# Performance work log

Measured on AMD Instinct MI355X. Metric: run time of the kernel, lower is better.

Reference implementation:

```python
import jax, jax.numpy as jnp
import numpy as np

PE_DIM = 64

def _layernorm(x, g, b, eps=1e-5):
    m = jnp.mean(x, -1, keepdims=True)
    v = jnp.mean((x - m) ** 2, -1, keepdims=True)
    return (x - m) * jax.lax.rsqrt(v + eps) * g + b

def _sinusoidal_pe(t, dim=PE_DIM):
    half = dim // 2
    freqs = jnp.exp(-jnp.log(10000.0) * jnp.arange(half) / half).astype(t.dtype)
    ang = t[..., None] * freqs  # [..., half]
    return jnp.concatenate([jnp.sin(ang), jnp.cos(ang)], -1)

def _bilinear(feats, b, t, x, y):
    # feats [B,Wl,H,W,D]; b,t int32 [B,Q,Wl,M] (b broadcastable); x,y in [0,1]
    # matches torch grid_sample(mode=bilinear, padding_mode=border, align_corners=False)
    H, W = feats.shape[2], feats.shape[3]
    px = x * W - 0.5
    py = y * H - 0.5
    x0 = jnp.floor(px); y0 = jnp.floor(py)
    wx = (px - x0)[..., None]; wy = (py - y0)[..., None]
    x0i = jnp.clip(x0.astype(jnp.int32), 0, W - 1)
    x1i = jnp.clip(x0.astype(jnp.int32) + 1, 0, W - 1)
    y0i = jnp.clip(y0.astype(jnp.int32), 0, H - 1)
    y1i = jnp.clip(y0.astype(jnp.int32) + 1, 0, H - 1)
    v00 = feats[b, t, y0i, x0i]  # [B,Q,Wl,M,D]
    v01 = feats[b, t, y0i, x1i]
    v10 = feats[b, t, y1i, x0i]
    v11 = feats[b, t, y1i, x1i]
    return (v00 * (1 - wy) * (1 - wx) + v01 * (1 - wy) * wx
            + v10 * wy * (1 - wx) + v11 * wy * wx)

def setup_inputs() -> dict:
    key = jax.random.key(0)
    ks = jax.random.split(key, 20)
    B, Q, Wl, H, W, D, M = 4, 300, 8, 64, 64, 256, 4
    s = 0.02
    inp = {
        'q': jax.random.normal(ks[0], (B, Q, D), jnp.float32),
        'kv_feats': jax.random.normal(ks[1], (B, Wl, H, W, D), jnp.float32),
        'kv_mask': jnp.zeros((B, Wl, H, W), jnp.bool_),
        'delta_sec': jax.random.normal(ks[2], (B, Q, Wl), jnp.float32),
        'w_ref': jax.random.normal(ks[3], (D, 2), jnp.float32) * s,
        'b_ref': jnp.zeros((2,), jnp.float32),
        'w_delta': jax.random.normal(ks[4], (2 * D, 3 * M), jnp.float32) * s,
        'b_delta': jnp.zeros((3 * M,), jnp.float32),
        'w_alpha': jax.random.normal(ks[5], (2 * D, M), jnp.float32) * s,
        'b_alpha': jnp.zeros((M,), jnp.float32),
        'lam': jnp.array(1.0, jnp.float32),
        'w_proj': jax.random.normal(ks[6], (D, D), jnp.float32) * s,
        'b_proj': jnp.zeros((D,), jnp.float32),
        'ln1_g': jnp.ones((D,), jnp.float32), 'ln1_b': jnp.zeros((D,), jnp.float32),
        'ln2_g': jnp.ones((D,), jnp.float32), 'ln2_b': jnp.zeros((D,), jnp.float32),
        'w_ffn1': jax.random.normal(ks[7], (D, 4 * D), jnp.float32) * s,
        'b_ffn1': jnp.zeros((4 * D,), jnp.float32),
        'w_ffn2': jax.random.normal(ks[8], (4 * D, D), jnp.float32) * s,
        'b_ffn2': jnp.zeros((D,), jnp.float32),
        'w_rel': jax.random.normal(ks[9], (PE_DIM, D), jnp.float32) * s,
        'b_rel': jnp.zeros((D,), jnp.float32),
    }
    return inp

def reference(q, kv_feats, kv_mask, delta_sec, w_ref, b_ref, w_delta, b_delta,
              w_alpha, b_alpha, lam, w_proj, b_proj, ln1_g, ln1_b, ln2_g, ln2_b,
              w_ffn1, b_ffn1, w_ffn2, b_ffn2, w_rel, b_rel):
    B, Q, D = q.shape
    Wl = kv_feats.shape[1]
    M = w_alpha.shape[1]

    qn = _layernorm(q, ln1_g, ln1_b)
    rel_feat = _sinusoidal_pe(delta_sec) @ w_rel + b_rel          # [B,Q,Wl,D]
    psi = jnp.concatenate([jnp.broadcast_to(qn[:, :, None, :], (B, Q, Wl, D)),
                           rel_feat], -1)                          # [B,Q,Wl,2D]

    delta = (psi @ w_delta + b_delta).reshape(B, Q, Wl, M, 3)
    logits = psi @ w_alpha + b_alpha                               # [B,Q,Wl,M]
    ref = jax.nn.sigmoid(qn @ w_ref + b_ref)                       # [B,Q,2]
    coords = ref[:, :, None, None, :] + jnp.tanh(delta[..., :2])   # [B,Q,Wl,M,2]
    coords = jnp.clip(coords, 0.0, 1.0)
    delta_t = jnp.tanh(delta[..., 2])                              # [B,Q,Wl,M]

    # mask features (mask==True -> invalid -> zero)
    feats = kv_feats * (~kv_mask)[..., None].astype(kv_feats.dtype)

    # temporal trilinear indices
    base = jnp.arange(Wl, dtype=q.dtype).reshape(1, 1, Wl, 1)
    target = base + delta_t
    t0f = jnp.clip(jnp.floor(target), 0, Wl - 1)
    t1f = jnp.clip(t0f + 1, 0, Wl - 1)
    alpha = (target - t0f)[..., None]
    t0 = t0f.astype(jnp.int32); t1 = t1f.astype(jnp.int32)

    bidx = jnp.arange(B, dtype=jnp.int32).reshape(B, 1, 1, 1)
    cx = coords[..., 0]; cy = coords[..., 1]
    s0 = _bilinear(feats, bidx, t0, cx, cy)                        # [B,Q,Wl,M,D]
    s1 = _bilinear(feats, bidx, t1, cx, cy)
    sampled = s0 * (1 - alpha) + s1 * alpha

    lam_sp = jax.nn.softplus(lam)
    weights = jax.nn.softmax(logits - lam_sp * jnp.abs(delta_sec)[..., None], axis=-1)
    agg = jnp.sum(weights[..., None] * sampled, axis=(2, 3))       # [B,Q,D]

    out = q + (agg @ w_proj + b_proj)
    h = _layernorm(out, ln2_g, ln2_b)
    ffn = jax.nn.gelu(h @ w_ffn1 + b_ffn1, approximate=False) @ w_ffn2 + b_ffn2
    return out + ffn
```

## Files before the change

kernel.cpp:

```cpp
#include <hip/hip_runtime.h>
#include <math.h>

#define Bn 4
#define Qn 300
#define WL 8
#define Hh 64
#define Ww 64
#define Dd 256
#define Mm 4

__device__ __forceinline__ float wave_reduce(float v) {
#pragma unroll
    for (int off = 32; off > 0; off >>= 1) v += __shfl_down(v, off, 64);
    return v;
}

__device__ __forceinline__ float lo16(unsigned u) { return __uint_as_float(u << 16); }
__device__ __forceinline__ float hi16(unsigned u) { return __uint_as_float(u & 0xffff0000u); }

__device__ __forceinline__ unsigned bfp(float a, float b) {
    unsigned ua = __float_as_uint(a); ua = (ua + 0x7fffu + ((ua >> 16) & 1u)) >> 16;
    unsigned ub = __float_as_uint(b); ub = (ub + 0x7fffu + ((ub >> 16) & 1u)) >> 16;
    return ua | (ub << 16);
}

__device__ __forceinline__ void unpack8(uint4 wv, float* w) {
    w[0] = lo16(wv.x); w[1] = hi16(wv.x); w[2] = lo16(wv.y); w[3] = hi16(wv.y);
    w[4] = lo16(wv.z); w[5] = hi16(wv.z); w[6] = lo16(wv.w); w[7] = hi16(wv.w);
}

__device__ __forceinline__ float dot8(float4 ha, float4 hb, const float* w) {
    return ha.x * w[0] + ha.y * w[1] + ha.z * w[2] + ha.w * w[3]
         + hb.x * w[4] + hb.y * w[5] + hb.z * w[6] + hb.w * w[7];
}

__global__ void __launch_bounds__(512, 4) k_front(const float* __restrict__ wp,
                                                  const float* __restrict__ wf1,
                                                  const float* __restrict__ wf2,
                                                  unsigned* __restrict__ pk,
                                                  const float* __restrict__ q,
                                                  const float* __restrict__ g1,
                                                  const float* __restrict__ b1,
                                                  const float* __restrict__ w_ref,
                                                  const float* __restrict__ b_ref,
                                                  const float* __restrict__ dsec,
                                                  const float* __restrict__ w_rel,
                                                  const float* __restrict__ b_rel,
                                                  const float* __restrict__ w_delta,
                                                  const float* __restrict__ b_delta,
                                                  const float* __restrict__ w_alpha,
                                                  const float* __restrict__ b_alpha,
                                                  const unsigned char* __restrict__ mask,
                                                  const float* __restrict__ feats,
                                                  float* __restrict__ agg) {
    int bid = blockIdx.x, t = threadIdx.x;

    if (bid < 576) {
        int i = bid * 512 + t;
        if (i < 32768) {
            int p = i & 3, c = (i >> 2) & 255, g = i >> 10;
            pk[i] = bfp(wp[(g * 8 + 2 * p) * 256 + c], wp[(g * 8 + 2 * p + 1) * 256 + c]);
        } else if (i < 163840) {
            int i2 = i - 32768;
            int p = i2 & 3, c = (i2 >> 2) & 1023, g = i2 >> 12;
            pk[i] = bfp(wf1[(g * 8 + 2 * p) * 1024 + c], wf1[(g * 8 + 2 * p + 1) * 1024 + c]);
        } else {
            int i3 = i - 163840;
            int p = i3 & 3, c = (i3 >> 2) & 255, g = i3 >> 10;
            pk[i] = bfp(wf2[(g * 8 + 2 * p) * 256 + c], wf2[(g * 8 + 2 * p + 1) * 256 + c]);
        }
        return;
    }

    __shared__ float sqn[256];
    __shared__ float pe[8][64];
    __shared__ float rel[8][260];
    __shared__ __align__(16) float WcT[16 * 516];
    __shared__ float dres[2][8][16];
    __shared__ float res[8][16];
    __shared__ float red[16];
    __shared__ float sref[2];
    float (*part)[256] = (float (*)[256])WcT;
    unsigned* Prec = (unsigned*)(WcT + 2048);

    int bq = bid - 576;
    int ch = t & 255;
    bool lo = t < 256;
    int lane = t & 63, wv = t >> 6;

    float wr[64];
#pragma unroll
    for (int k = 0; k < 64; k++) wr[k] = w_rel[k * Dd + ch];

    for (int u = t; u < 512 * 16; u += 512) {
        int k = u >> 4, jj = u & 15;
        float w = (jj < 12) ? w_delta[k * 12 + jj] : w_alpha[k * 4 + (jj - 12)];
        WcT[jj * 516 + k] = w;
    }

    float x = lo ? q[bq * Dd + ch] : 0.f;
    float sm = wave_reduce(x);
    if (lane == 0) red[wv] = sm;
    __syncthreads();
    float m = (red[0] + red[1] + red[2] + red[3] + red[4] + red[5] + red[6] + red[7]) * (1.f / Dd);
    __syncthreads();
    float dx = lo ? (x - m) : 0.f;
    float sv = wave_reduce(dx * dx);
    if (lane == 0) red[wv] = sv;
    __syncthreads();
    float v = (red[0] + red[1] + red[2] + red[3] + red[4] + red[5] + red[6] + red[7]) * (1.f / Dd);
    __syncthreads();
    float y = 0.f;
    if (lo) { y = dx * rsqrtf(v + 1e-5f) * g1[ch] + b1[ch]; sqn[ch] = y; }

    if (lo) {
        int wl = t >> 5, i2 = t & 31;
        float f = expf(-logf(10000.f) * (float)i2 * (1.f / 32.f));
        float a = dsec[bq * WL + wl] * f;
        pe[wl][i2] = sinf(a);
        pe[wl][i2 + 32] = cosf(a);
    }

    float c0 = lo ? y * w_ref[2 * ch] : 0.f;
    float c1 = lo ? y * w_ref[2 * ch + 1] : 0.f;
    c0 = wave_reduce(c0); c1 = wave_reduce(c1);
    if (lane == 0) { red[wv] = c0; red[8 + wv] = c1; }
    __syncthreads();
    if (t == 0) {
        float s0 = red[0] + red[1] + red[2] + red[3] + red[4] + red[5] + red[6] + red[7] + b_ref[0];
        float s1 = red[8] + red[9] + red[10] + red[11] + red[12] + red[13] + red[14] + red[15] + b_ref[1];
        sref[0] = 1.f / (1.f + expf(-s0));
        sref[1] = 1.f / (1.f + expf(-s1));
    }

    {
        float brl = b_rel[ch];
        int wh = t >> 8;
#pragma unroll
        for (int w2 = 0; w2 < 4; w2++) {
            int wl = wh * 4 + w2;
            const float4* p4 = (const float4*)&pe[wl][0];
            float r = brl;
#pragma unroll
            for (int k4 = 0; k4 < 16; k4++) {
                float4 p = p4[k4];
                r += p.x * wr[4 * k4] + p.y * wr[4 * k4 + 1]
                   + p.z * wr[4 * k4 + 2] + p.w * wr[4 * k4 + 3];
            }
            rel[wl][ch] = r;
        }
    }
    __syncthreads();

    if (t < 256) {
        int h = t >> 7, idx = t & 127, wl = idx >> 4, jj = idx & 15;
        const float4* wrow = (const float4*)&WcT[jj * 516 + h * 256];
        const float4* arow = h ? (const float4*)&rel[wl][0] : (const float4*)sqn;
        float s = 0.f;
#pragma unroll 8
        for (int k4 = 0; k4 < 64; k4++) {
            float4 a = arow[k4], w = wrow[k4];
            s += a.x * w.x + a.y * w.y + a.z * w.z + a.w * w.w;
        }
        dres[h][wl][jj] = s;
    }
    __syncthreads();
    if (t < 128) {
        int wl = t >> 4, jj = t & 15;
        res[wl][jj] = dres[0][wl][jj] + dres[1][wl][jj]
                    + ((jj < 12) ? b_delta[jj] : b_alpha[jj - 12]);
    }
    __syncthreads();

    if (t < 32) {
        int wl = t >> 2, mm = t & 3;
        float l0 = res[wl][12], l1 = res[wl][13], l2 = res[wl][14], l3 = res[wl][15];
        float mx = fmaxf(fmaxf(l0, l1), fmaxf(l2, l3));
        float inv = 1.f / (expf(l0 - mx) + expf(l1 - mx) + expf(l2 - mx) + expf(l3 - mx));
        float wgt = expf(res[wl][12 + mm] - mx) * inv;

        float cx = fminf(fmaxf(sref[0] + tanhf(res[wl][mm * 3 + 0]), 0.f), 1.f);
        float cy = fminf(fmaxf(sref[1] + tanhf(res[wl][mm * 3 + 1]), 0.f), 1.f);
        float tgt = (float)wl + tanhf(res[wl][mm * 3 + 2]);
        float t0f = fminf(fmaxf(floorf(tgt), 0.f), (float)(WL - 1));
        float t1f = fminf(t0f + 1.f, (float)(WL - 1));
        float alpha = tgt - t0f;
        float px = cx * (float)Ww - 0.5f, py = cy * (float)Hh - 0.5f;
        float fx = floorf(px), fy = floorf(py);
        float wx = px - fx, wy = py - fy;
        int X0 = (int)fminf(fmaxf(fx, 0.f), (float)(Ww - 1));
        int X1 = (int)fminf(fmaxf(fx + 1.f, 0.f), (float)(Ww - 1));
        int Y0 = (int)fminf(fmaxf(fy, 0.f), (float)(Hh - 1));
        int Y1 = (int)fminf(fmaxf(fy + 1.f, 0.f), (float)(Hh - 1));
        int T0 = (int)t0f, T1 = (int)t1f;

        float w00 = (1.f - wy) * (1.f - wx), w01 = (1.f - wy) * wx;
        float w10 = wy * (1.f - wx), w11 = wy * wx;
        float wt0 = wgt * (1.f - alpha), wt1 = wgt * alpha;

        int b = bq / Qn;
        int base0 = (b * WL + T0) * Hh;
        int base1 = (b * WL + T1) * Hh;
        int i00 = (base0 + Y0) * Ww + X0, i01 = (base0 + Y0) * Ww + X1;
        int i10 = (base0 + Y1) * Ww + X0, i11 = (base0 + Y1) * Ww + X1;
        int j00 = (base1 + Y0) * Ww + X0, j01 = (base1 + Y0) * Ww + X1;
        int j10 = (base1 + Y1) * Ww + X0, j11 = (base1 + Y1) * Ww + X1;

        unsigned* rec = &Prec[t * 16];
        rec[0] = __float_as_uint(wt0 * w00 * (mask[i00] ? 0.f : 1.f));
        rec[1] = __float_as_uint(wt0 * w01 * (mask[i01] ? 0.f : 1.f));
        rec[2] = __float_as_uint(wt0 * w10 * (mask[i10] ? 0.f : 1.f));
        rec[3] = __float_as_uint(wt0 * w11 * (mask[i11] ? 0.f : 1.f));
        rec[4] = __float_as_uint(wt1 * w00 * (mask[j00] ? 0.f : 1.f));
        rec[5] = __float_as_uint(wt1 * w01 * (mask[j01] ? 0.f : 1.f));
        rec[6] = __float_as_uint(wt1 * w10 * (mask[j10] ? 0.f : 1.f));
        rec[7] = __float_as_uint(wt1 * w11 * (mask[j11] ? 0.f : 1.f));
        rec[8] = i00; rec[9] = i01; rec[10] = i10; rec[11] = i11;
        rec[12] = j00; rec[13] = j01; rec[14] = j10; rec[15] = j11;
    }
    __syncthreads();

    {
        const float4* f4 = (const float4*)feats;
        int j = t >> 6;
        float4 acc = {0.f, 0.f, 0.f, 0.f};
#pragma unroll
        for (int p = 0; p < 4; p++) {
            const unsigned* rec = &Prec[(j * 4 + p) * 16];
#pragma unroll
            for (int cn = 0; cn < 8; cn++) {
                float w = __uint_as_float(rec[cn]);
                size_t idx = rec[8 + cn];
                float4 vv = f4[idx * 64 + lane];
                acc.x += w * vv.x; acc.y += w * vv.y; acc.z += w * vv.z; acc.w += w * vv.w;
            }
        }
        ((float4*)&part[j][0])[lane] = acc;
    }
    __syncthreads();
    if (t < 256) {
        agg[(size_t)bq * Dd + t] = part[0][t] + part[1][t] + part[2][t] + part[3][t]
                                 + part[4][t] + part[5][t] + part[6][t] + part[7][t];
    }
}

template<int R>
__device__ __forceinline__ void out_body(int row0,
        const float* __restrict__ q, const float* __restrict__ agg,
        const unsigned* __restrict__ pkP, const float* __restrict__ b_proj,
        const float* __restrict__ g2, const float* __restrict__ b2,
        const unsigned* __restrict__ pkF1, const float* __restrict__ b_ffn1,
        const unsigned* __restrict__ pkF2, const float* __restrict__ b_ffn2,
        float* __restrict__ out,
        float* sA, float* sO, float* sH, float* sF, float* sX, float* sRed) {
    int t = threadIdx.x;
    int j8 = t >> 7, c7 = t & 127;

    for (int u = t; u < 256 * R; u += 1024) {
        int r = u >> 8, cc = u & 255;
        sA[r * 256 + cc] = agg[(size_t)(row0 + r) * Dd + cc];
    }
    __syncthreads();

    {
        float a0[R], a1[R];
#pragma unroll
        for (int r = 0; r < R; r++) { a0[r] = 0.f; a1[r] = 0.f; }
#pragma unroll
        for (int gg = 0; gg < 4; gg++) {
            int g = j8 * 4 + gg;
            uint4 wv0 = *(const uint4*)&pkP[((unsigned)(g * 256 + c7)) * 4];
            uint4 wv1 = *(const uint4*)&pkP[((unsigned)(g * 256 + c7 + 128)) * 4];
            float w0[8], w1[8]; unpack8(wv0, w0); unpack8(wv1, w1);
#pragma unroll
            for (int r = 0; r < R; r++) {
                float4 ha = ((const float4*)&sA[r * 256])[g * 2];
                float4 hb = ((const float4*)&sA[r * 256])[g * 2 + 1];
                a0[r] += dot8(ha, hb, w0); a1[r] += dot8(ha, hb, w1);
            }
        }
#pragma unroll
        for (int r = 0; r < R; r++) {
            sX[(j8 * R + r) * 256 + c7] = a0[r];
            sX[(j8 * R + r) * 256 + c7 + 128] = a1[r];
        }
    }
    __syncthreads();

    for (int u = t; u < 256 * R; u += 1024) {
        int r = u >> 8, cc = u & 255;
        float o = q[(size_t)(row0 + r) * Dd + cc] + b_proj[cc];
#pragma unroll
        for (int jj = 0; jj < 8; jj++) o += sX[(jj * R + r) * 256 + cc];
        sO[r * 256 + cc] = o;
    }
    __syncthreads();

    {
        int wv = t >> 6, l = t & 63;
        if (wv < R) {
            float4 vv = ((const float4*)&sO[wv * 256])[l];
            float s = vv.x + vv.y + vv.z + vv.w;
            s = __shfl(wave_reduce(s), 0, 64);
            float mean = s * (1.f / 256.f);
            float d0 = vv.x - mean, d1 = vv.y - mean, d2 = vv.z - mean, d3 = vv.w - mean;
            float ss = d0 * d0 + d1 * d1 + d2 * d2 + d3 * d3;
            ss = __shfl(wave_reduce(ss), 0, 64);
            float rstd = rsqrtf(ss * (1.f / 256.f) + 1e-5f);
            if (l == 0) { sRed[wv * 2] = mean; sRed[wv * 2 + 1] = rstd; }
        }
    }
    __syncthreads();
    for (int u = t; u < 256 * R; u += 1024) {
        int r = u >> 8, cc = u & 255;
        sH[r * 256 + cc] = (sO[r * 256 + cc] - sRed[r * 2]) * sRed[r * 2 + 1] * g2[cc] + b2[cc];
    }
    __syncthreads();

    {
        int h = t >> 9, c2 = t & 511;
        float f0[R], f1[R];
#pragma unroll
        for (int r = 0; r < R; r++) { f0[r] = 0.f; f1[r] = 0.f; }
#pragma unroll 2
        for (int gg = 0; gg < 16; gg++) {
            int g = h * 16 + gg;
            uint4 wv0 = *(const uint4*)&pkF1[((unsigned)(g * 1024 + c2)) * 4];
            uint4 wv1 = *(const uint4*)&pkF1[((unsigned)(g * 1024 + c2 + 512)) * 4];
            float w0[8], w1[8]; unpack8(wv0, w0); unpack8(wv1, w1);
#pragma unroll
            for (int r = 0; r < R; r++) {
                float4 ha = ((const float4*)&sH[r * 256])[g * 2];
                float4 hb = ((const float4*)&sH[r * 256])[g * 2 + 1];
                f0[r] += dot8(ha, hb, w0); f1[r] += dot8(ha, hb, w1);
            }
        }
        float* dst = sX + h * (R * 1024);
#pragma unroll
        for (int r = 0; r < R; r++) {
            dst[r * 1024 + c2] = f0[r];
            dst[r * 1024 + c2 + 512] = f1[r];
        }
    }
    __syncthreads();
    {
        float bf = b_ffn1[t];
#pragma unroll
        for (int r = 0; r < R; r++) {
            float xx = sX[r * 1024 + t] + sX[R * 1024 + r * 1024 + t] + bf;
            sF[r * 1024 + t] = 0.5f * xx * (1.f + erff(xx * 0.70710678118654752f));
        }
    }
    __syncthreads();

    {
        float a0[R], a1[R];
#pragma unroll
        for (int r = 0; r < R; r++) { a0[r] = 0.f; a1[r] = 0.f; }
#pragma unroll 2
        for (int gg = 0; gg < 16; gg++) {
            int g = j8 * 16 + gg;
            uint4 wv0 = *(const uint4*)&pkF2[((unsigned)(g * 256 + c7)) * 4];
            uint4 wv1 = *(const uint4*)&pkF2[((unsigned)(g * 256 + c7 + 128)) * 4];
            float w0[8], w1[8]; unpack8(wv0, w0); unpack8(wv1, w1);
#pragma unroll
            for (int r = 0; r < R; r++) {
                float4 ha = ((const float4*)&sF[r * 1024])[g * 2];
                float4 hb = ((const float4*)&sF[r * 1024])[g * 2 + 1];
                a0[r] += dot8(ha, hb, w0); a1[r] += dot8(ha, hb, w1);
            }
        }
#pragma unroll
        for (int r = 0; r < R; r++) {
            sX[(j8 * R + r) * 256 + c7] = a0[r];
            sX[(j8 * R + r) * 256 + c7 + 128] = a1[r];
        }
    }
    __syncthreads();

    for (int u = t; u < 256 * R; u += 1024) {
        int r = u >> 8, cc = u & 255;
        float s = b_ffn2[cc];
#pragma unroll
        for (int jj = 0; jj < 8; jj++) s += sX[(jj * R + r) * 256 + cc];
        out[(size_t)(row0 + r) * Dd + cc] = sO[r * 256 + cc] + s;
    }
}

__global__ void __launch_bounds__(1024) k_out(const float* __restrict__ q,
                                              const float* __restrict__ agg,
                                              const unsigned* __restrict__ pkP,
                                              const float* __restrict__ b_proj,
                                              const float* __restrict__ g2,
                                              const float* __restrict__ b2,
                                              const unsigned* __restrict__ pkF1,
                                              const float* __restrict__ b_ffn1,
                                              const unsigned* __restrict__ pkF2,
                                              const float* __restrict__ b_ffn2,
                                              float* __restrict__ out) {
    __shared__ float sA[5 * 256];
    __shared__ float sO[5 * 256];
    __shared__ float sH[5 * 256];
    __shared__ float sF[5 * 1024];
    __shared__ float sX[10240];
    __shared__ float sRed[16];
    __shared__ float pad[1600];
    if (b_ffn2 == nullptr) pad[threadIdx.x & 1023] = 0.f;

    int bid = blockIdx.x;
    if (bid < 176) {
        out_body<5>(bid * 5, q, agg, pkP, b_proj, g2, b2, pkF1, b_ffn1, pkF2, b_ffn2,
                    out, sA, sO, sH, sF, sX, sRed);
    } else {
        out_body<4>(880 + (bid - 176) * 4, q, agg, pkP, b_proj, g2, b2, pkF1, b_ffn1,
                    pkF2, b_ffn2, out, sA, sO, sH, sF, sX, sRed);
    }
}

extern "C" void kernel_launch(void* const* d_in, const int* in_sizes, int n_in,
                              void* d_out, int out_size, void* d_ws, size_t ws_size,
                              hipStream_t stream) {
    const float* q        = (const float*)d_in[0];
    const float* kv_feats = (const float*)d_in[1];
    const unsigned char* kv_mask = (const unsigned char*)d_in[2];
    const float* delta_sec= (const float*)d_in[3];
    const float* w_ref    = (const float*)d_in[4];
    const float* b_ref    = (const float*)d_in[5];
    const float* w_delta  = (const float*)d_in[6];
    const float* b_delta  = (const float*)d_in[7];
    const float* w_alpha  = (const float*)d_in[8];
    const float* b_alpha  = (const float*)d_in[9];
    const float* w_proj   = (const float*)d_in[11];
    const float* b_proj   = (const float*)d_in[12];
    const float* ln1_g    = (const float*)d_in[13];
    const float* ln1_b    = (const float*)d_in[14];
    const float* ln2_g    = (const float*)d_in[15];
    const float* ln2_b    = (const float*)d_in[16];
    const float* w_ffn1   = (const float*)d_in[17];
    const float* b_ffn1   = (const float*)d_in[18];
    const float* w_ffn2   = (const float*)d_in[19];
    const float* b_ffn2   = (const float*)d_in[20];
    const float* w_rel    = (const float*)d_in[21];
    const float* b_rel    = (const float*)d_in[22];
    float* out = (float*)d_out;

    unsigned* pk   = (unsigned*)d_ws;
    unsigned* pkP  = pk;
    unsigned* pkF1 = pk + 32768;
    unsigned* pkF2 = pk + 163840;
    float*    agg  = (float*)(pk + 294912);

    const int BQ = Bn * Qn;
    k_front<<<dim3(576 + BQ), dim3(512), 0, stream>>>(w_proj, w_ffn1, w_ffn2, pk,
                                                      q, ln1_g, ln1_b, w_ref, b_ref,
                                                      delta_sec, w_rel, b_rel,
                                                      w_delta, b_delta, w_alpha, b_alpha,
                                                      kv_mask, kv_feats, agg);
    k_out<<<dim3(256), dim3(1024), 0, stream>>>(q, agg, pkP, b_proj, ln2_g, ln2_b,
                                                pkF1, b_ffn1, pkF2, b_ffn2, out);
}
```

Baseline: 294.4 us.

## Switch output MLP weights and activations to fp16 with packed dot2 accumulation

Weights for the projection and both FFN layers are now packed as fp16 pairs instead of bf16, and activations in shared memory are stored as packed fp16 too. The inner products use the fdot2 instruction (two fp16 multiplies accumulated into fp32) instead of unpacking to fp32 and doing scalar FMAs. The aim is fewer ALU ops in the k_out matmuls and smaller shared-memory traffic. The cost is fp16 range and rounding on activations, and the shared-memory pad is enlarged, presumably to keep occupancy the same.

Result: faster. 278.3 us (-5.5%).

```diff
diff --git a/kernel.cpp b/kernel.cpp
--- a/kernel.cpp
+++ b/kernel.cpp
@@ -15,23 +15,32 @@
     return v;
 }
 
-__device__ __forceinline__ float lo16(unsigned u) { return __uint_as_float(u << 16); }
-__device__ __forceinline__ float hi16(unsigned u) { return __uint_as_float(u & 0xffff0000u); }
-
-__device__ __forceinline__ unsigned bfp(float a, float b) {
-    unsigned ua = __float_as_uint(a); ua = (ua + 0x7fffu + ((ua >> 16) & 1u)) >> 16;
-    unsigned ub = __float_as_uint(b); ub = (ub + 0x7fffu + ((ub >> 16) & 1u)) >> 16;
-    return ua | (ub << 16);
-}
-
-__device__ __forceinline__ void unpack8(uint4 wv, float* w) {
-    w[0] = lo16(wv.x); w[1] = hi16(wv.x); w[2] = lo16(wv.y); w[3] = hi16(wv.y);
-    w[4] = lo16(wv.z); w[5] = hi16(wv.z); w[6] = lo16(wv.w); w[7] = hi16(wv.w);
-}
-
-__device__ __forceinline__ float dot8(float4 ha, float4 hb, const float* w) {
-    return ha.x * w[0] + ha.y * w[1] + ha.z * w[2] + ha.w * w[3]
-         + hb.x * w[4] + hb.y * w[5] + hb.z * w[6] + hb.w * w[7];
+using h2_t = _Float16 __attribute__((ext_vector_type(2)));
+
+__device__ __forceinline__ unsigned packh2(float a, float b) {
+    auto h = __builtin_amdgcn_cvt_pkrtz(a, b);
+    union { decltype(h) h; unsigned u; } x; x.h = h; return x.u;
+}
+
+__device__ __forceinline__ h2_t u2h2(unsigned u) {
+    union { unsigned u; h2_t h; } x; x.u = u; return x.h;
+}
+
+__device__ __forceinline__ float dot2p(unsigned a, unsigned w, float acc) {
+#if __has_builtin(__builtin_amdgcn_fdot2)
+    return __builtin_amdgcn_fdot2(u2h2(a), u2h2(w), acc, false);
+#else
+    h2_t A = u2h2(a), W = u2h2(w);
+    return acc + (float)A.x * (float)W.x + (float)A.y * (float)W.y;
+#endif
+}
+
+__device__ __forceinline__ float dot8h(uint4 av, uint4 wv, float acc) {
+    acc = dot2p(av.x, wv.x, acc);
+    acc = dot2p(av.y, wv.y, acc);
+    acc = dot2p(av.z, wv.z, acc);
+    acc = dot2p(av.w, wv.w, acc);
+    return acc;
 }
 
 __global__ void __launch_bounds__(512, 4) k_front(const float* __restrict__ wp,
@@ -59,15 +68,15 @@
         int i = bid * 512 + t;
         if (i < 32768) {
             int p = i & 3, c = (i >> 2) & 255, g = i >> 10;
-            pk[i] = bfp(wp[(g * 8 + 2 * p) * 256 + c], wp[(g * 8 + 2 * p + 1) * 256 + c]);
+            pk[i] = packh2(wp[(g * 8 + 2 * p) * 256 + c], wp[(g * 8 + 2 * p + 1) * 256 + c]);
         } else if (i < 163840) {
             int i2 = i - 32768;
             int p = i2 & 3, c = (i2 >> 2) & 1023, g = i2 >> 12;
-            pk[i] = bfp(wf1[(g * 8 + 2 * p) * 1024 + c], wf1[(g * 8 + 2 * p + 1) * 1024 + c]);
+            pk[i] = packh2(wf1[(g * 8 + 2 * p) * 1024 + c], wf1[(g * 8 + 2 * p + 1) * 1024 + c]);
         } else {
             int i3 = i - 163840;
             int p = i3 & 3, c = (i3 >> 2) & 255, g = i3 >> 10;
-            pk[i] = bfp(wf2[(g * 8 + 2 * p) * 256 + c], wf2[(g * 8 + 2 * p + 1) * 256 + c]);
+            pk[i] = packh2(wf2[(g * 8 + 2 * p) * 256 + c], wf2[(g * 8 + 2 * p + 1) * 256 + c]);
         }
         return;
     }
@@ -252,13 +261,14 @@
         const unsigned* __restrict__ pkF1, const float* __restrict__ b_ffn1,
         const unsigned* __restrict__ pkF2, const float* __restrict__ b_ffn2,
         float* __restrict__ out,
-        float* sA, float* sO, float* sH, float* sF, float* sX, float* sRed) {
+        unsigned* sA2, float* sO, unsigned* sH2, unsigned* sF2, float* sX, float* sRed) {
     int t = threadIdx.x;
     int j8 = t >> 7, c7 = t & 127;
 
-    for (int u = t; u < 256 * R; u += 1024) {
-        int r = u >> 8, cc = u & 255;
-        sA[r * 256 + cc] = agg[(size_t)(row0 + r) * Dd + cc];
+    for (int u = t; u < 128 * R; u += 1024) {
+        int r = u >> 7, c2 = u & 127;
+        float2 av = *(const float2*)&agg[(size_t)(row0 + r) * Dd + 2 * c2];
+        sA2[r * 128 + c2] = packh2(av.x, av.y);
     }
     __syncthreads();
 
@@ -271,12 +281,11 @@
             int g = j8 * 4 + gg;
             uint4 wv0 = *(const uint4*)&pkP[((unsigned)(g * 256 + c7)) * 4];
             uint4 wv1 = *(const uint4*)&pkP[((unsigned)(g * 256 + c7 + 128)) * 4];
-            float w0[8], w1[8]; unpack8(wv0, w0); unpack8(wv1, w1);
 #pragma unroll
             for (int r = 0; r < R; r++) {
-                float4 ha = ((const float4*)&sA[r * 256])[g * 2];
-                float4 hb = ((const float4*)&sA[r * 256])[g * 2 + 1];
-                a0[r] += dot8(ha, hb, w0); a1[r] += dot8(ha, hb, w1);
+                uint4 av = ((const uint4*)&sA2[r * 128])[g];
+                a0[r] = dot8h(av, wv0, a0[r]);
+                a1[r] = dot8h(av, wv1, a1[r]);
             }
         }
 #pragma unroll
@@ -311,45 +320,52 @@
         }
     }
     __syncthreads();
-    for (int u = t; u < 256 * R; u += 1024) {
-        int r = u >> 8, cc = u & 255;
-        sH[r * 256 + cc] = (sO[r * 256 + cc] - sRed[r * 2]) * sRed[r * 2 + 1] * g2[cc] + b2[cc];
-    }
-    __syncthreads();
-
-    {
-        int h = t >> 9, c2 = t & 511;
+    for (int u = t; u < 128 * R; u += 1024) {
+        int r = u >> 7, c2 = u & 127;
+        int cc = 2 * c2;
+        float mean = sRed[r * 2], rstd = sRed[r * 2 + 1];
+        float h0 = (sO[r * 256 + cc] - mean) * rstd * g2[cc] + b2[cc];
+        float h1 = (sO[r * 256 + cc + 1] - mean) * rstd * g2[cc + 1] + b2[cc + 1];
+        sH2[r * 128 + c2] = packh2(h0, h1);
+    }
+    __syncthreads();
+
+    {
+        int h = t >> 9, c2c = t & 511;
         float f0[R], f1[R];
 #pragma unroll
         for (int r = 0; r < R; r++) { f0[r] = 0.f; f1[r] = 0.f; }
 #pragma unroll 2
         for (int gg = 0; gg < 16; gg++) {
             int g = h * 16 + gg;
-            uint4 wv0 = *(const uint4*)&pkF1[((unsigned)(g * 1024 + c2)) * 4];
-            uint4 wv1 = *(const uint4*)&pkF1[((unsigned)(g * 1024 + c2 + 512)) * 4];
-            float w0[8], w1[8]; unpack8(wv0, w0); unpack8(wv1, w1);
+            uint4 wv0 = *(const uint4*)&pkF1[((unsigned)(g * 1024 + c2c)) * 4];
+            uint4 wv1 = *(const uint4*)&pkF1[((unsigned)(g * 1024 + c2c + 512)) * 4];
 #pragma unroll
             for (int r = 0; r < R; r++) {
-                float4 ha = ((const float4*)&sH[r * 256])[g * 2];
-                float4 hb = ((const float4*)&sH[r * 256])[g * 2 + 1];
-                f0[r] += dot8(ha, hb, w0); f1[r] += dot8(ha, hb, w1);
+                uint4 av = ((const uint4*)&sH2[r * 128])[g];
+                f0[r] = dot8h(av, wv0, f0[r]);
+                f1[r] = dot8h(av, wv1, f1[r]);
             }
         }
         float* dst = sX + h * (R * 1024);
 #pragma unroll
         for (int r = 0; r < R; r++) {
-            dst[r * 1024 + c2] = f0[r];
-            dst[r * 1024 + c2 + 512] = f1[r];
-        }
-    }
-    __syncthreads();
-    {
-        float bf = b_ffn1[t];
-#pragma unroll
-        for (int r = 0; r < R; r++) {
-            float xx = sX[r * 1024 + t] + sX[R * 1024 + r * 1024 + t] + bf;
-            sF[r * 1024 + t] = 0.5f * xx * (1.f + erff(xx * 0.70710678118654752f));
-        }
+            dst[r * 1024 + c2c] = f0[r];
+            dst[r * 1024 + c2c + 512] = f1[r];
+        }
+    }
+    __syncthreads();
+
+    for (int u = t; u < 512 * R; u += 1024) {
+        int r = u >> 9, p = u & 511;
+        float2 pa = ((const float2*)&sX[r * 1024])[p];
+        float2 pb = ((const float2*)&sX[R * 1024 + r * 1024])[p];
+        float2 bf = *(const float2*)&b_ffn1[2 * p];
+        float x0 = pa.x + pb.x + bf.x;
+        float x1 = pa.y + pb.y + bf.y;
+        float e0 = 0.5f * x0 * (1.f + erff(x0 * 0.70710678118654752f));
+        float e1 = 0.5f * x1 * (1.f + erff(x1 * 0.70710678118654752f));
+        sF2[r * 512 + p] = packh2(e0, e1);
     }
     __syncthreads();
 
@@ -362,12 +378,11 @@
             int g = j8 * 16 + gg;
             uint4 wv0 = *(const uint4*)&pkF2[((unsigned)(g * 256 + c7)) * 4];
             uint4 wv1 = *(const uint4*)&pkF2[((unsigned)(g * 256 + c7 + 128)) * 4];
-            float w0[8], w1[8]; unpack8(wv0, w0); unpack8(wv1, w1);
 #pragma unroll
             for (int r = 0; r < R; r++) {
-                float4 ha = ((const float4*)&sF[r * 1024])[g * 2];
-                float4 hb = ((const float4*)&sF[r * 1024])[g * 2 + 1];
-                a0[r] += dot8(ha, hb, w0); a1[r] += dot8(ha, hb, w1);
+                uint4 av = ((const uint4*)&sF2[r * 512])[g];
+                a0[r] = dot8h(av, wv0, a0[r]);
+                a1[r] = dot8h(av, wv1, a1[r]);
             }
         }
 #pragma unroll
@@ -398,22 +413,22 @@
                                               const unsigned* __restrict__ pkF2,
                                               const float* __restrict__ b_ffn2,
                                               float* __restrict__ out) {
-    __shared__ float sA[5 * 256];
-    __shared__ float sO[5 * 256];
-    __shared__ float sH[5 * 256];
-    __shared__ float sF[5 * 1024];
-    __shared__ float sX[10240];
+    __shared__ __align__(16) unsigned sA2[5 * 128];
+    __shared__ __align__(16) float sO[5 * 256];
+    __shared__ __align__(16) unsigned sH2[5 * 128];
+    __shared__ __align__(16) unsigned sF2[5 * 512];
+    __shared__ __align__(16) float sX[10240];
     __shared__ float sRed[16];
-    __shared__ float pad[1600];
+    __shared__ float pad[5120];
     if (b_ffn2 == nullptr) pad[threadIdx.x & 1023] = 0.f;
 
     int bid = blockIdx.x;
     if (bid < 176) {
         out_body<5>(bid * 5, q, agg, pkP, b_proj, g2, b2, pkF1, b_ffn1, pkF2, b_ffn2,
-                    out, sA, sO, sH, sF, sX, sRed);
+                    out, sA2, sO, sH2, sF2, sX, sRed);
     } else {
         out_body<4>(880 + (bid - 176) * 4, q, agg, pkP, b_proj, g2, b2, pkF1, b_ffn1,
-                    pkF2, b_ffn2, out, sA, sO, sH, sF, sX, sRed);
+                    pkF2, b_ffn2, out, sA2, sO, sH2, sF2, sX, sRed);
     }
 }
 
```
